# Kernel tuning notes

Hardware: AMD Instinct MI355X
Metric: run time of the kernel (lower is better)

The kernel has to match this reference:

```python
import jax, jax.numpy as jnp
import numpy as np

N_NODES = 100000
N_EDGES = 3200000
IN_F = 256
OUT_F = 128
NEG_SLOPE = 0.2


def setup_inputs() -> dict:
    key = jax.random.key(0)
    k1, k2, k3, k4, k5 = jax.random.split(key, 5)
    features = jax.random.normal(k1, (N_NODES, IN_F), dtype=jnp.float32)
    # xavier-uniform-ish linear weight [out, in]
    limit = float(np.sqrt(6.0 / (IN_F + OUT_F)))
    weight = jax.random.uniform(k2, (OUT_F, IN_F), dtype=jnp.float32, minval=-limit, maxval=limit)
    edge_vals = jax.random.uniform(k3, (N_EDGES,), dtype=jnp.float32)
    edge_rows = jax.random.randint(k4, (N_EDGES,), 0, N_NODES, dtype=jnp.int32)
    edge_cols = jax.random.randint(k5, (N_EDGES,), 0, N_NODES, dtype=jnp.int32)
    return {"features": features, "weight": weight, "edge_vals": edge_vals,
            "edge_rows": edge_rows, "edge_cols": edge_cols}


def reference(features, weight, edge_vals, edge_rows, edge_cols):
    # support = LeakyReLU(features @ W^T)   (active=True path)
    support = jax.nn.leaky_relu(jnp.einsum('ni,oi->no', features, weight), NEG_SLOPE)
    # output = spmm(adj, support): out[r] += v_e * support[c_e]
    gathered = support[edge_cols] * edge_vals[:, None]   # [E, out]
    out = jax.ops.segment_sum(gathered, edge_rows, num_segments=N_NODES)
    return out
```

## Files before the change

kernel.cpp:

```cpp
#include <hip/hip_runtime.h>
#include <hip/hip_bf16.h>

#define N_NODES 100000
#define N_EDGES 3200000
#define IN_F 256
#define OUT_F 128
#define NEG_SLOPE 0.2f
#define GB 782
#define CHUNK 4096
#define NPB 782
#define GCAP 4608
#define SCAP 2560

typedef short s16x8 __attribute__((ext_vector_type(8)));
typedef float f32x4 __attribute__((ext_vector_type(4)));

__device__ __forceinline__ unsigned short f2bf(float f) {
    __bf16 h = (__bf16)f;
    return __builtin_bit_cast(unsigned short, h);
}
__device__ __forceinline__ float bf2f(unsigned short u) {
    unsigned int x = ((unsigned int)u) << 16;
    return __builtin_bit_cast(float, x);
}

__global__ void wcvt_kernel(const float* __restrict__ w, unsigned short* __restrict__ wb) {
    int i = (blockIdx.x * blockDim.x + threadIdx.x) * 4;
    if (i >= OUT_F * IN_F) return;
    float4 v = *(const float4*)(w + i);
    ushort4 o;
    o.x = f2bf(v.x); o.y = f2bf(v.y); o.z = f2bf(v.z); o.w = f2bf(v.w);
    *(ushort4*)(wb + i) = o;
}

__global__ __launch_bounds__(256) void gemm_kernel(
    const float* __restrict__ feat, const unsigned short* __restrict__ wb,
    unsigned short* __restrict__ sup) {
    int wid  = threadIdx.x >> 6;
    int lane = threadIdx.x & 63;
    long m0 = ((long)blockIdx.x * 4 + wid) * 16;
    if (m0 >= N_NODES) return;
    int quad = lane >> 4;
    int l16  = lane & 15;
    int kq   = quad * 8;

    const float* arow = feat + (m0 + l16) * IN_F + kq;

    f32x4 acc[8];
#pragma unroll
    for (int nt = 0; nt < 8; ++nt) acc[nt] = (f32x4){0.f, 0.f, 0.f, 0.f};

#pragma unroll
    for (int k0 = 0; k0 < IN_F; k0 += 32) {
        float4 a0 = *(const float4*)(arow + k0);
        float4 a1 = *(const float4*)(arow + k0 + 4);
        s16x8 a;
        a[0] = (short)f2bf(a0.x); a[1] = (short)f2bf(a0.y);
        a[2] = (short)f2bf(a0.z); a[3] = (short)f2bf(a0.w);
        a[4] = (short)f2bf(a1.x); a[5] = (short)f2bf(a1.y);
        a[6] = (short)f2bf(a1.z); a[7] = (short)f2bf(a1.w);
        const unsigned short* wp = wb + l16 * IN_F + k0 + kq;
#pragma unroll
        for (int nt = 0; nt < 8; ++nt) {
            s16x8 b = *(const s16x8*)(wp + (long)nt * 16 * IN_F);
            acc[nt] = __builtin_amdgcn_mfma_f32_16x16x32_bf16(a, b, acc[nt], 0, 0, 0);
        }
    }

    int crow = (int)m0 + quad * 4;
#pragma unroll
    for (int nt = 0; nt < 8; ++nt) {
#pragma unroll
        for (int r = 0; r < 4; ++r) {
            float v = acc[nt][r];
            v = (v > 0.f) ? v : (NEG_SLOPE * v);
            sup[(long)(crow + r) * OUT_F + nt * 16 + l16] = f2bf(v);
        }
    }
}

__global__ __launch_bounds__(256) void hist_kernel(const int* __restrict__ rows,
                                                   int* __restrict__ cnt) {
    __shared__ int lh[GB];
    for (int s = threadIdx.x; s < GB; s += 256) lh[s] = 0;
    __syncthreads();
    int e0 = blockIdx.x * CHUNK;
    int m = N_EDGES - e0; if (m > CHUNK) m = CHUNK;
    for (int k = threadIdx.x; k < m; k += 256)
        atomicAdd(&lh[rows[e0 + k] >> 7], 1);
    __syncthreads();
    for (int s = threadIdx.x; s < GB; s += 256)
        if (lh[s]) atomicAdd(&cnt[s], lh[s]);
}

__global__ __launch_bounds__(256) void scan_kernel(const int* __restrict__ cnt,
                                                   int* __restrict__ off,
                                                   int* __restrict__ cursor) {
    __shared__ int st[256];
    int t = threadIdx.x;
    int base = t * 4;
    int v[4]; int sum = 0;
#pragma unroll
    for (int k = 0; k < 4; ++k) {
        int s = base + k;
        v[k] = (s < GB) ? cnt[s] : 0;
        sum += v[k];
    }
    st[t] = sum;
    __syncthreads();
    for (int o = 1; o < 256; o <<= 1) {
        int x = (t >= o) ? st[t - o] : 0;
        __syncthreads();
        st[t] += x;
        __syncthreads();
    }
    int run = st[t] - sum;
#pragma unroll
    for (int k = 0; k < 4; ++k) {
        int s = base + k;
        if (s < GB) { off[s] = run; cursor[s] = run; }
        run += v[k];
    }
}

__global__ __launch_bounds__(256) void mscatter_kernel(const int* __restrict__ rows,
    const int* __restrict__ cols, const float* __restrict__ vals,
    int* __restrict__ cursor, uint2* __restrict__ ed) {
    __shared__ uint2 stage[CHUNK];
    __shared__ unsigned short sbkt[CHUNK];
    __shared__ int lhist[GB];
    __shared__ int lcnt[GB];
    __shared__ int lbase[GB];
    __shared__ int st[256];
    int t = threadIdx.x;
    for (int s = t; s < GB; s += 256) lhist[s] = 0;
    __syncthreads();
    int e0 = blockIdx.x * CHUNK;
    int m = N_EDGES - e0; if (m > CHUNK) m = CHUNK;

    int rk[16]; int bkrl[16]; unsigned cw[16], vw[16];
#pragma unroll
    for (int k = 0; k < 16; ++k) {
        int i = k * 256 + t;
        if (i < m) {
            int e = e0 + i;
            int r = rows[e];
            int b = r >> 7;
            bkrl[k] = (b << 7) | (r & 127);
            cw[k] = (unsigned)cols[e];
            vw[k] = __builtin_bit_cast(unsigned, vals[e]);
            rk[k] = atomicAdd(&lhist[b], 1);
        }
    }
    __syncthreads();
    for (int s = t; s < GB; s += 256) lcnt[s] = lhist[s];
    int base = t * 4; int sum = 0; int hv[4];
#pragma unroll
    for (int k = 0; k < 4; ++k) { int s = base + k; hv[k] = (s < GB) ? lhist[s] : 0; sum += hv[k]; }
    st[t] = sum; __syncthreads();
    for (int o = 1; o < 256; o <<= 1) {
        int x = (t >= o) ? st[t - o] : 0;
        __syncthreads();
        st[t] += x;
        __syncthreads();
    }
    int run = st[t] - sum;
#pragma unroll
    for (int k = 0; k < 4; ++k) { int s = base + k; if (s < GB) lhist[s] = run; run += hv[k]; }
    __syncthreads();
    for (int s = t; s < GB; s += 256)
        if (lcnt[s]) lbase[s] = atomicAdd(&cursor[s], lcnt[s]);
#pragma unroll
    for (int k = 0; k < 16; ++k) {
        int i = k * 256 + t;
        if (i < m) {
            int b  = bkrl[k] >> 7;
            int rl = bkrl[k] & 127;
            int pos = lhist[b] + rk[k];
            stage[pos].x = ((unsigned)rl << 17) | cw[k];
            stage[pos].y = vw[k];
            sbkt[pos] = (unsigned short)b;
        }
    }
    __syncthreads();
    for (int i = t; i < m; i += 256) {
        int b = sbkt[i];
        ed[lbase[b] + (i - lhist[b])] = stage[i];
    }
}

__global__ __launch_bounds__(512) void gather_kernel(const uint2* __restrict__ ed,
    const int* __restrict__ off, const int* __restrict__ cnt,
    const unsigned short* __restrict__ sup, float* __restrict__ out) {
    __shared__ uint2 stage[SCAP];
    __shared__ int h[64];
    __shared__ int bs[64];
    __shared__ int cur[64];
    int t = threadIdx.x;
    int bkt  = blockIdx.x >> 1;
    int half = blockIdx.x & 1;
    if (t < 64) h[t] = 0;
    __syncthreads();
    int n = cnt[bkt]; if (n > GCAP) n = GCAP;
    int start = off[bkt];
    const uint2* p = ed + start;

    uint2 er[9];
#pragma unroll
    for (int k = 0; k < 9; ++k) {
        int i = k * 512 + t;
        if (i < n) er[k] = p[i];
    }
#pragma unroll
    for (int k = 0; k < 9; ++k) {
        int i = k * 512 + t;
        if (i < n) {
            int rl = er[k].x >> 17;
            if ((rl >> 6) == half) atomicAdd(&h[rl & 63], 1);
        }
    }
    __syncthreads();

    if (t < 64) bs[t] = h[t];
    __syncthreads();
    for (int o = 1; o < 64; o <<= 1) {
        int v = 0;
        if (t < 64 && t >= o) v = bs[t - o];
        __syncthreads();
        if (t < 64) bs[t] += v;
        __syncthreads();
    }
    if (t < 64) {
        int excl = bs[t] - h[t];
        bs[t] = excl;
        cur[t] = excl;
    }
    __syncthreads();

#pragma unroll
    for (int k = 0; k < 9; ++k) {
        int i = k * 512 + t;
        if (i < n) {
            int rl = er[k].x >> 17;
            if ((rl >> 6) == half) {
                int pos = atomicAdd(&cur[rl & 63], 1);
                if (pos < SCAP) stage[pos] = er[k];
            }
        }
    }
    __syncthreads();

    int wid = t >> 6, lane = t & 63;
    long rowbase = (long)bkt * 128 + half * 64;

#define PROC(E) {                                                            \
        int col = (E).x & 0x1FFFF;                                           \
        float v = __builtin_bit_cast(float, (E).y);                          \
        ushort2 s2 = *(const ushort2*)(sup + (long)col * OUT_F + lane * 2);  \
        a0 += v * bf2f(s2.x); a1 += v * bf2f(s2.y);                          \
    }

    for (int rr = 0; rr < 8; ++rr) {
        int lr = wid * 8 + rr;
        int s0 = bs[lr];
        int m  = h[lr];
        if (s0 + m > SCAP) m = SCAP - s0;
        float a0 = 0.f, a1 = 0.f;
        int i = 0;
        for (; i + 8 <= m; i += 8) {
            uint2 e0 = stage[s0 + i],     e1 = stage[s0 + i + 1];
            uint2 e2 = stage[s0 + i + 2], e3 = stage[s0 + i + 3];
            uint2 e4 = stage[s0 + i + 4], e5 = stage[s0 + i + 5];
            uint2 e6 = stage[s0 + i + 6], e7 = stage[s0 + i + 7];
            PROC(e0); PROC(e1); PROC(e2); PROC(e3);
            PROC(e4); PROC(e5); PROC(e6); PROC(e7);
        }
        for (; i < m; ++i) { uint2 e0 = stage[s0 + i]; PROC(e0); }
        long grow = rowbase + lr;
        if (grow < N_NODES) {
            float2 f; f.x = a0; f.y = a1;
            *(float2*)(out + grow * OUT_F + lane * 2) = f;
        }
    }
#undef PROC
}

extern "C" void kernel_launch(void* const* d_in, const int* in_sizes, int n_in,
                              void* d_out, int out_size, void* d_ws, size_t ws_size,
                              hipStream_t stream) {
    const float* feat  = (const float*)d_in[0];
    const float* w     = (const float*)d_in[1];
    const float* evals = (const float*)d_in[2];
    const int*   erows = (const int*)d_in[3];
    const int*   ecols = (const int*)d_in[4];
    float* out = (float*)d_out;

    char* p = (char*)d_ws;
    unsigned short* wb  = (unsigned short*)p;  p += 65536;
    unsigned short* sup = (unsigned short*)p;  p += (size_t)N_NODES * OUT_F * 2;
    int* cnt    = (int*)p;                     p += 8192;
    int* off    = (int*)p;                     p += 8192;
    int* cursor = (int*)p;                     p += 8192;
    uint2* ed   = (uint2*)p;

    hipMemsetAsync(cnt, 0, GB * sizeof(int), stream);

    wcvt_kernel<<<(OUT_F * IN_F / 4 + 255) / 256, 256, 0, stream>>>(w, wb);

    int gemm_blocks = (N_NODES / 16 + 3) / 4;
    gemm_kernel<<<gemm_blocks, 256, 0, stream>>>(feat, wb, sup);

    hist_kernel<<<NPB, 256, 0, stream>>>(erows, cnt);
    scan_kernel<<<1, 256, 0, stream>>>(cnt, off, cursor);
    mscatter_kernel<<<NPB, 256, 0, stream>>>(erows, ecols, evals, cursor, ed);
    gather_kernel<<<GB * 2, 512, 0, stream>>>(ed, off, cnt, sup, out);
}
```

Baseline: 419.9 us.

## Prepack weights in MFMA order, add nontemporal loads/stores, unroll gather by 16

The weight conversion kernel now writes bf16 weights in the exact per-lane MFMA fragment order, so the GEMM reads B fragments contiguously (lane*8) instead of strided rows. Nontemporal loads and stores are added for streaming data: feature reads, edge cols and vals, staged edge reads and the output writes, to reduce cache pollution. The gather loop gains a 16-way unrolled stage that issues more independent support-row loads in flight. These are several unrelated tweaks. The extra unrolling raises register pressure, and nontemporal hints may hurt any data that does get reused.

Result: faster. 391.9 us (-6.7%).

```diff
diff --git a/kernel.cpp b/kernel.cpp
--- a/kernel.cpp
+++ b/kernel.cpp
@@ -14,6 +14,8 @@
 
 typedef short s16x8 __attribute__((ext_vector_type(8)));
 typedef float f32x4 __attribute__((ext_vector_type(4)));
+typedef float f32x2v __attribute__((ext_vector_type(2)));
+typedef unsigned u32x2 __attribute__((ext_vector_type(2)));
 
 __device__ __forceinline__ unsigned short f2bf(float f) {
     __bf16 h = (__bf16)f;
@@ -25,12 +27,21 @@
 }
 
 __global__ void wcvt_kernel(const float* __restrict__ w, unsigned short* __restrict__ wb) {
-    int i = (blockIdx.x * blockDim.x + threadIdx.x) * 4;
-    if (i >= OUT_F * IN_F) return;
-    float4 v = *(const float4*)(w + i);
-    ushort4 o;
-    o.x = f2bf(v.x); o.y = f2bf(v.y); o.z = f2bf(v.z); o.w = f2bf(v.w);
-    *(ushort4*)(wb + i) = o;
+    int t = blockIdx.x * blockDim.x + threadIdx.x;
+    if (t >= (OUT_F / 16) * (IN_F / 32) * 64) return;
+    int lane = t & 63;
+    int nt   = (t >> 6) & 7;
+    int kit  = t >> 9;
+    int l16  = lane & 15;
+    int quad = lane >> 4;
+    const float* src = w + (nt * 16 + l16) * IN_F + kit * 32 + quad * 8;
+    float4 v0 = *(const float4*)src;
+    float4 v1 = *(const float4*)(src + 4);
+    ushort4 o0, o1;
+    o0.x = f2bf(v0.x); o0.y = f2bf(v0.y); o0.z = f2bf(v0.z); o0.w = f2bf(v0.w);
+    o1.x = f2bf(v1.x); o1.y = f2bf(v1.y); o1.z = f2bf(v1.z); o1.w = f2bf(v1.w);
+    *(ushort4*)(wb + t * 8)     = o0;
+    *(ushort4*)(wb + t * 8 + 4) = o1;
 }
 
 __global__ __launch_bounds__(256) void gemm_kernel(
@@ -52,17 +63,17 @@
 
 #pragma unroll
     for (int k0 = 0; k0 < IN_F; k0 += 32) {
-        float4 a0 = *(const float4*)(arow + k0);
-        float4 a1 = *(const float4*)(arow + k0 + 4);
+        f32x4 a0 = __builtin_nontemporal_load((const f32x4*)(arow + k0));
+        f32x4 a1 = __builtin_nontemporal_load((const f32x4*)(arow + k0 + 4));
         s16x8 a;
-        a[0] = (short)f2bf(a0.x); a[1] = (short)f2bf(a0.y);
-        a[2] = (short)f2bf(a0.z); a[3] = (short)f2bf(a0.w);
-        a[4] = (short)f2bf(a1.x); a[5] = (short)f2bf(a1.y);
-        a[6] = (short)f2bf(a1.z); a[7] = (short)f2bf(a1.w);
-        const unsigned short* wp = wb + l16 * IN_F + k0 + kq;
+        a[0] = (short)f2bf(a0[0]); a[1] = (short)f2bf(a0[1]);
+        a[2] = (short)f2bf(a0[2]); a[3] = (short)f2bf(a0[3]);
+        a[4] = (short)f2bf(a1[0]); a[5] = (short)f2bf(a1[1]);
+        a[6] = (short)f2bf(a1[2]); a[7] = (short)f2bf(a1[3]);
+        const unsigned short* wp = wb + (k0 >> 5) * 4096 + lane * 8;
 #pragma unroll
         for (int nt = 0; nt < 8; ++nt) {
-            s16x8 b = *(const s16x8*)(wp + (long)nt * 16 * IN_F);
+            s16x8 b = *(const s16x8*)(wp + nt * 512);
             acc[nt] = __builtin_amdgcn_mfma_f32_16x16x32_bf16(a, b, acc[nt], 0, 0, 0);
         }
     }
@@ -147,8 +158,8 @@
             int r = rows[e];
             int b = r >> 7;
             bkrl[k] = (b << 7) | (r & 127);
-            cw[k] = (unsigned)cols[e];
-            vw[k] = __builtin_bit_cast(unsigned, vals[e]);
+            cw[k] = (unsigned)__builtin_nontemporal_load(cols + e);
+            vw[k] = __builtin_bit_cast(unsigned, __builtin_nontemporal_load(vals + e));
             rk[k] = atomicAdd(&lhist[b], 1);
         }
     }
@@ -209,7 +220,10 @@
 #pragma unroll
     for (int k = 0; k < 9; ++k) {
         int i = k * 512 + t;
-        if (i < n) er[k] = p[i];
+        if (i < n) {
+            u32x2 v = __builtin_nontemporal_load((const u32x2*)(p + i));
+            er[k].x = v[0]; er[k].y = v[1];
+        }
     }
 #pragma unroll
     for (int k = 0; k < 9; ++k) {
@@ -267,6 +281,13 @@
         if (s0 + m > SCAP) m = SCAP - s0;
         float a0 = 0.f, a1 = 0.f;
         int i = 0;
+        for (; i + 16 <= m; i += 16) {
+            uint2 e[16];
+#pragma unroll
+            for (int k = 0; k < 16; ++k) e[k] = stage[s0 + i + k];
+#pragma unroll
+            for (int k = 0; k < 16; ++k) PROC(e[k]);
+        }
         for (; i + 8 <= m; i += 8) {
             uint2 e0 = stage[s0 + i],     e1 = stage[s0 + i + 1];
             uint2 e2 = stage[s0 + i + 2], e3 = stage[s0 + i + 3];
@@ -278,8 +299,8 @@
         for (; i < m; ++i) { uint2 e0 = stage[s0 + i]; PROC(e0); }
         long grow = rowbase + lr;
         if (grow < N_NODES) {
-            float2 f; f.x = a0; f.y = a1;
-            *(float2*)(out + grow * OUT_F + lane * 2) = f;
+            f32x2v f; f[0] = a0; f[1] = a1;
+            __builtin_nontemporal_store(f, (f32x2v*)(out + grow * OUT_F + lane * 2));
         }
     }
 #undef PROC
@@ -305,7 +326,7 @@
 
     hipMemsetAsync(cnt, 0, GB * sizeof(int), stream);
 
-    wcvt_kernel<<<(OUT_F * IN_F / 4 + 255) / 256, 256, 0, stream>>>(w, wb);
+    wcvt_kernel<<<16, 256, 0, stream>>>(w, wb);
 
     int gemm_blocks = (N_NODES / 16 + 3) / 4;
     gemm_kernel<<<gemm_blocks, 256, 0, stream>>>(feat, wb, sup);
```
